# Kernel tuning notes

Hardware: AMD Instinct MI355X
Metric: run time of the kernel (lower is better)

The kernel has to match this reference:

```python
import jax, jax.numpy as jnp
import numpy as np
import math

BN_EPS = 1e-5
LOG20 = math.log(20.0)

def conv1x1(w, x):
    # w: [O, C], x: [B, C, N] -> [B, O, N]
    return jnp.einsum('oc,bcn->bon', w, x)

def bn_silu(x, g, b, m, v):
    # inference-mode BatchNorm1d over channel dim, then SiLU
    y = (x - m[None, :, None]) * (g / jnp.sqrt(v + BN_EPS))[None, :, None] + b[None, :, None]
    return y * jax.nn.sigmoid(y)

def setup_inputs() -> dict:
    key = jax.random.key(0)
    ks = jax.random.split(key, 16)
    B, N, M = 8, 4096, 4096
    f32 = jnp.float32
    d = {
        'pcd_f': jax.random.normal(ks[0], (B, 1152, N), f32),
        'img_f': jax.random.normal(ks[1], (B, 1024, M), f32),
        'q_w': jax.random.normal(ks[2], (1024, 1152), f32) * 0.02,
        'k_w': jax.random.normal(ks[3], (1024, 1024), f32) * 0.02,
        'v_w': jax.random.normal(ks[4], (1024, 1024), f32) * 0.02,
        'skip_w': jax.random.normal(ks[5], (1024, 1152), f32) * 0.02,
        'c1_w': jax.random.normal(ks[6], (256, 1024), f32) * 0.03,
        'bn1_g': jnp.ones((256,), f32),
        'bn1_b': jnp.zeros((256,), f32),
        'bn1_m': jax.random.normal(ks[7], (256,), f32) * 0.1,
        'bn1_v': jnp.ones((256,), f32) + 0.1 * jax.random.uniform(ks[8], (256,)),
        'c2_w': jax.random.normal(ks[9], (64, 256), f32) * 0.06,
        'bn2_g': jnp.ones((64,), f32),
        'bn2_b': jnp.zeros((64,), f32),
        'bn2_m': jax.random.normal(ks[10], (64,), f32) * 0.1,
        'bn2_v': jnp.ones((64,), f32) + 0.1 * jax.random.uniform(ks[11], (64,)),
        'c3_w': jax.random.normal(ks[12], (1, 64), f32) * 0.1,
        'c3_b': jnp.zeros((1,), f32),
    }
    return d

def reference(pcd_f, img_f, q_w, k_w, v_w, skip_w, c1_w, bn1_g, bn1_b, bn1_m, bn1_v,
              c2_w, bn2_g, bn2_b, bn2_m, bn2_v, c3_w, c3_b):
    q = conv1x1(q_w, pcd_f)                       # [B, 1024, N]
    k = conv1x1(k_w, img_f)                       # [B, 1024, M]
    v = conv1x1(v_w, img_f)                       # [B, 1024, M]
    scale = math.sqrt(q.shape[1])                 # sqrt(C) = 32
    energy = jnp.einsum('bcn,bcm->bnm', q, k) / scale
    attn = jax.nn.softmax(energy, axis=-1)        # [B, N, M]
    x = jnp.einsum('bnm,bcm->bcn', attn, v)       # [B, 1024, N]
    x = conv1x1(skip_w, pcd_f) + x
    x = bn_silu(conv1x1(c1_w, x), bn1_g, bn1_b, bn1_m, bn1_v)   # [B, 256, N]
    x = bn_silu(conv1x1(c2_w, x), bn2_g, bn2_b, bn2_m, bn2_v)   # [B, 64, N]
    x = conv1x1(c3_w, x) + c3_b[None, :, None]    # [B, 1, N]
    x = x[:, 0, :]                                # squeeze channel -> [B, N]
    return jax.nn.sigmoid(x * LOG20)              # 1/(1+20^-x)
```

## Files before the change

### kernel.cpp

```cpp
#include <hip/hip_runtime.h>

#define LOG20F 2.9957322735539909f
#define AS1 __attribute__((address_space(1)))
#define AS3 __attribute__((address_space(3)))

typedef __attribute__((ext_vector_type(4))) short short4v;
typedef __attribute__((ext_vector_type(8))) short short8;
typedef __attribute__((ext_vector_type(8))) __bf16 bf16x8;
typedef __attribute__((ext_vector_type(4))) float f32x4;

__device__ __forceinline__ short f2bf(float f) {
  unsigned u = __float_as_uint(f);
  u = u + 0x7fffu + ((u >> 16) & 1u);
  return (short)(u >> 16);
}
__device__ __forceinline__ float bf2f(short s) {
  return __uint_as_float(((unsigned)(unsigned short)s) << 16);
}

__device__ __forceinline__ void xcd_map(int& bx, int& by, int& bz) {
  int gx = gridDim.x, gy = gridDim.y;
  int nwg = gx * gy * (int)gridDim.z;
  int lin = bx + gx * (by + gy * bz);
  int q = nwg >> 3, r = nwg & 7;
  int xcd = lin & 7, idx = lin >> 3;
  int wg = (xcd < r ? xcd * (q + 1) : r * (q + 1) + (xcd - r) * q) + idx;
  int per_z = gx * gy;
  bz = wg / per_z;
  int rz = wg - bz * per_z;
  if ((gx & 3) == 0 && (gy & 3) == 0) {
    int nstx = gx >> 2;
    int st = rz >> 4, w = rz & 15;
    bx = ((st % nstx) << 2) + (w & 3);
    by = ((st / nstx) << 2) + (w >> 2);
  } else {
    bx = rz % gx;
    by = rz / gx;
  }
}

template <int EPI>
__global__ __launch_bounds__(512, 2) void gemm8(
    const short* __restrict__ A, const short* __restrict__ B,
    short* __restrict__ C, const short* __restrict__ addp,
    float* __restrict__ rs,
    int K, int lda, int ldb, int ldc, int ldadd,
    long abatch, long bbatch, long cbatch, long addbatch, float scale)
{
  __shared__ __align__(16) short lA[2][256 * 64];
  __shared__ __align__(16) short lB[2][256 * 64];
  __shared__ float rsum_l[256];

  int bx = blockIdx.x, by = blockIdx.y, bz = blockIdx.z;
  xcd_map(bx, by, bz);

  const int tid = threadIdx.x;
  const int lane = tid & 63, wid = tid >> 6;
  const int wr = wid >> 2, wc = wid & 3;

  const long bm = (long)bx * 256, bn = (long)by * 256;
  const short* Ab = A + (long)bz * abatch + bm * lda;
  const short* Bb = B + (long)bz * bbatch + bn * ldb;

  f32x4 acc[8][4] = {};

  const int NKT = K >> 6;

  auto stageA = [&](int buf, int kt) {
    int k0 = kt << 6;
#pragma unroll
    for (int i = 0; i < 4; ++i) {
      int idx = i * 512 + tid;
      int row = idx >> 3, ch = idx & 7;
      int chs = ch ^ (row & 7);
      __builtin_amdgcn_global_load_lds(
          (const AS1 void*)(Ab + (long)row * lda + k0 + chs * 8),
          (AS3 void*)(&lA[buf][row * 64 + ch * 8]), 16, 0, 0);
    }
  };
  auto stageB = [&](int buf, int kt) {
    int k0 = kt << 6;
#pragma unroll
    for (int i = 0; i < 4; ++i) {
      int idx = i * 512 + tid;
      int row = idx >> 3, ch = idx & 7;
      int chs = ch ^ (row & 7);
      __builtin_amdgcn_global_load_lds(
          (const AS1 void*)(Bb + (long)row * ldb + k0 + chs * 8),
          (AS3 void*)(&lB[buf][row * 64 + ch * 8]), 16, 0, 0);
    }
  };

  const int rr = lane & 15, cl = lane >> 4;
  bf16x8 bfr[4][2], af[4][2];

  auto loadA2 = [&](int buf, int h) {
#pragma unroll
    for (int f = 0; f < 4; ++f) {
      int row = wr * 128 + h * 64 + f * 16 + rr;
#pragma unroll
      for (int kk = 0; kk < 2; ++kk) {
        int pch = (kk * 4 + cl) ^ (row & 7);
        af[f][kk] = *(const bf16x8*)&lA[buf][row * 64 + pch * 8];
      }
    }
  };
  auto loadB2 = [&](int buf) {
#pragma unroll
    for (int ni = 0; ni < 4; ++ni) {
      int row = wc * 64 + ni * 16 + rr;
#pragma unroll
      for (int kk = 0; kk < 2; ++kk) {
        int pch = (kk * 4 + cl) ^ (row & 7);
        bfr[ni][kk] = *(const bf16x8*)&lB[buf][row * 64 + pch * 8];
      }
    }
  };

#define BAR() __builtin_amdgcn_s_barrier()
#define LGKM0() asm volatile("s_waitcnt lgkmcnt(0)" ::: "memory")
#define MFMA_H(h)                                                        \
  do {                                                                   \
    __builtin_amdgcn_s_setprio(1);                                       \
    _Pragma("unroll")                                                    \
    for (int f = 0; f < 4; ++f)                                          \
      _Pragma("unroll")                                                  \
      for (int ni = 0; ni < 4; ++ni)                                     \
        _Pragma("unroll")                                                \
        for (int kk = 0; kk < 2; ++kk)                                   \
          acc[(h) * 4 + f][ni] = __builtin_amdgcn_mfma_f32_16x16x32_bf16(\
              af[f][kk], bfr[ni][kk], acc[(h) * 4 + f][ni], 0, 0, 0);    \
    __builtin_amdgcn_s_setprio(0);                                       \
  } while (0)

  stageB(0, 0); stageA(0, 0); stageB(1, 1);
  asm volatile("s_waitcnt vmcnt(4)" ::: "memory");
  BAR();

  for (int t2 = 0; t2 < NKT; t2 += 2) {
    const bool more = (t2 + 2 < NKT);
    stageA(1, t2 + 1);
    loadB2(0); loadA2(0, 0);
    BAR(); LGKM0(); MFMA_H(0); BAR();
    if (more) stageB(0, t2 + 2);
    loadA2(0, 1);
    if (more) { asm volatile("s_waitcnt vmcnt(4)" ::: "memory"); }
    else      { asm volatile("s_waitcnt vmcnt(0)" ::: "memory"); }
    BAR(); LGKM0(); MFMA_H(1); BAR();
    if (more) stageA(0, t2 + 2);
    loadB2(1); loadA2(1, 0);
    BAR(); LGKM0(); MFMA_H(0); BAR();
    if (more) stageB(1, t2 + 3);
    loadA2(1, 1);
    if (more) { asm volatile("s_waitcnt vmcnt(4)" ::: "memory"); }
    else      { asm volatile("s_waitcnt vmcnt(0)" ::: "memory"); }
    BAR(); LGKM0(); MFMA_H(1); BAR();
  }
#undef BAR
#undef LGKM0
#undef MFMA_H

  if constexpr (EPI == 2) {
    if (tid < 256) rsum_l[tid] = 0.f;
    __syncthreads();
#pragma unroll
    for (int mi = 0; mi < 8; ++mi) {
      int lrow0 = wr * 128 + (mi >> 2) * 64 + (mi & 3) * 16 + (cl << 2);
#pragma unroll
      for (int r = 0; r < 4; ++r) {
        float part = 0.f;
#pragma unroll
        for (int ni = 0; ni < 4; ++ni) {
          long col = bn + wc * 64 + ni * 16 + rr;
          float e = __expf(acc[mi][ni][r] * scale);
          C[(long)bz * cbatch + (bm + lrow0 + r) * ldc + col] = f2bf(e);
          part += e;
        }
        part += __shfl_xor(part, 1);
        part += __shfl_xor(part, 2);
        part += __shfl_xor(part, 4);
        part += __shfl_xor(part, 8);
        if (rr == 0) atomicAdd(&rsum_l[lrow0 + r], part);
      }
    }
    __syncthreads();
    if (tid < 256) atomicAdd(&rs[(long)bz * 4096 + bm + tid], rsum_l[tid]);
  } else {
#pragma unroll
    for (int mi = 0; mi < 8; ++mi) {
      long row0 = bm + wr * 128 + (mi >> 2) * 64 + (mi & 3) * 16 + (cl << 2);
      float inv[4];
      if constexpr (EPI == 1) {
#pragma unroll
        for (int r = 0; r < 4; ++r)
          inv[r] = 1.f / rs[(long)bz * 4096 + row0 + r];
      }
#pragma unroll
      for (int ni = 0; ni < 4; ++ni) {
        long col = bn + wc * 64 + ni * 16 + rr;
#pragma unroll
        for (int r = 0; r < 4; ++r) {
          long off = (long)bz * cbatch + (row0 + r) * ldc + col;
          float v = acc[mi][ni][r] * scale;
          if constexpr (EPI == 1)
            v = v * inv[r] +
                bf2f(addp[(long)bz * addbatch + (row0 + r) * ldadd + col]);
          C[off] = f2bf(v);
        }
      }
    }
  }
}

__device__ __forceinline__ int swz32(int row, int ch) {
  return row * 32 + ((ch ^ ((row >> 1) & 3)) << 3);
}

template <int BM, int BN, int WR, int WC, int EPI>
__global__ __launch_bounds__(WR * WC * 64, 4) void gemm_bt(
    const short* __restrict__ A, const short* __restrict__ B,
    short* __restrict__ C, const short* __restrict__ addp,
    const float* __restrict__ sc, const float* __restrict__ sh,
    int K, int lda, int ldb, int ldc,
    long abatch, long bbatch, long cbatch, float scale)
{
  constexpr int NTH = WR * WC * 64;
  constexpr int WM = BM / WR, WN = BN / WC;
  constexpr int MR = WM / 16, NR = WN / 16;
  constexpr int CA = (BM * 4) / NTH, CB = (BN * 4) / NTH;

  __shared__ __align__(16) short lA[2][BM * 32];
  __shared__ __align__(16) short lB[2][BN * 32];

  int bx = blockIdx.x, by = blockIdx.y, bz = blockIdx.z;
  xcd_map(bx, by, bz);

  const int tid = threadIdx.x;
  const int lane = tid & 63, wid = tid >> 6;
  const int wr = wid / WC, wc = wid % WC;

  const long bm = (long)bx * BM, bn = (long)by * BN;
  const short* Ab = A + (long)bz * abatch + bm * lda;
  const short* Bb = B + (long)bz * bbatch + bn * ldb;

  f32x4 acc[MR][NR] = {};

  auto stage = [&](int buf, int k0) {
#pragma unroll
    for (int i = 0; i < CA; ++i) {
      int idx = i * NTH + tid, row = idx >> 2, ch = idx & 3;
      int chs = ch ^ ((row >> 1) & 3);
      __builtin_amdgcn_global_load_lds(
          (const AS1 void*)(Ab + (long)row * lda + k0 + chs * 8),
          (AS3 void*)(&lA[buf][idx * 8]), 16, 0, 0);
    }
#pragma unroll
    for (int i = 0; i < CB; ++i) {
      int idx = i * NTH + tid, row = idx >> 2, ch = idx & 3;
      int chs = ch ^ ((row >> 1) & 3);
      __builtin_amdgcn_global_load_lds(
          (const AS1 void*)(Bb + (long)row * ldb + k0 + chs * 8),
          (AS3 void*)(&lB[buf][idx * 8]), 16, 0, 0);
    }
  };

  const int NT = K >> 5;
  stage(0, 0);
  __syncthreads();
  int cur = 0;
  for (int t = 0; t < NT; ++t) {
    if (t + 1 < NT) stage(cur ^ 1, (t + 1) << 5);
    const int ch = lane >> 4, rrow = lane & 15;
    bf16x8 af[MR], bfr[NR];
#pragma unroll
    for (int mi = 0; mi < MR; ++mi) {
      int row = wr * WM + mi * 16 + rrow;
      af[mi] = *(const bf16x8*)&lA[cur][swz32(row, ch)];
    }
#pragma unroll
    for (int ni = 0; ni < NR; ++ni) {
      int row = wc * WN + ni * 16 + rrow;
      bfr[ni] = *(const bf16x8*)&lB[cur][swz32(row, ch)];
    }
    __builtin_amdgcn_s_setprio(1);
#pragma unroll
    for (int mi = 0; mi < MR; ++mi)
#pragma unroll
      for (int ni = 0; ni < NR; ++ni)
        acc[mi][ni] = __builtin_amdgcn_mfma_f32_16x16x32_bf16(
            af[mi], bfr[ni], acc[mi][ni], 0, 0, 0);
    __builtin_amdgcn_s_setprio(0);
    __syncthreads();
    cur ^= 1;
  }

#pragma unroll
  for (int mi = 0; mi < MR; ++mi) {
    long row0 = bm + wr * WM + mi * 16 + ((lane >> 4) << 2);
#pragma unroll
    for (int ni = 0; ni < NR; ++ni) {
      long col = bn + wc * WN + ni * 16 + (lane & 15);
#pragma unroll
      for (int r = 0; r < 4; ++r) {
        long off = (long)bz * cbatch + (row0 + r) * ldc + col;
        float v = acc[mi][ni][r] * scale;
        if constexpr (EPI == 1) v += bf2f(addp[off]);
        if constexpr (EPI == 2) {
          float y = v * sc[col] + sh[col];
          v = y / (1.f + __expf(-y));
        }
        C[off] = f2bf(v);
      }
    }
  }
}

__global__ __launch_bounds__(256) void transpose_cvt(
    const float* __restrict__ in, short* __restrict__ out, int C, int N)
{
  __shared__ float tile[32][33];
  int n0 = blockIdx.x * 32, c0 = blockIdx.y * 32;
  long z = (long)blockIdx.z * C * N;
  int tx = threadIdx.x & 31, ty = threadIdx.x >> 5;
#pragma unroll
  for (int r = 0; r < 4; ++r) {
    int cc = ty + r * 8;
    tile[cc][tx] = in[z + (long)(c0 + cc) * N + n0 + tx];
  }
  __syncthreads();
#pragma unroll
  for (int r = 0; r < 4; ++r) {
    int nn = ty + r * 8;
    out[z + (long)(n0 + nn) * C + c0 + tx] = f2bf(tile[tx][nn]);
  }
}

__global__ __launch_bounds__(256) void cvt_bf16(
    const float* __restrict__ in, short* __restrict__ out, long n)
{
  long i = ((long)blockIdx.x * 256 + threadIdx.x) * 4;
  if (i >= n) return;
  const float* p = in + i;
  short4v s;
  s[0] = f2bf(p[0]); s[1] = f2bf(p[1]); s[2] = f2bf(p[2]); s[3] = f2bf(p[3]);
  *(short4v*)(out + i) = s;
}

__global__ void bn_prep(const float* g1, const float* b1, const float* m1, const float* v1,
                        const float* g2, const float* b2, const float* m2, const float* v2,
                        float* s1, float* t1, float* s2, float* t2)
{
  int i = threadIdx.x;
  if (i < 256) { float s = g1[i] * rsqrtf(v1[i] + 1e-5f); s1[i] = s; t1[i] = b1[i] - m1[i] * s; }
  if (i < 64)  { float s = g2[i] * rsqrtf(v2[i] + 1e-5f); s2[i] = s; t2[i] = b2[i] - m2[i] * s; }
}

__global__ __launch_bounds__(256) void zerof(float* __restrict__ p, int n)
{
  int i = blockIdx.x * 256 + threadIdx.x;
  if (i < n) p[i] = 0.f;
}

__global__ __launch_bounds__(256) void c3_out(
    const short* __restrict__ y2, const float* __restrict__ w,
    const float* __restrict__ bias, float* __restrict__ o, int total)
{
  int i = blockIdx.x * 256 + threadIdx.x;
  if (i >= total) return;
  const short8* r = (const short8*)(y2 + (long)i * 64);
  float acc = 0.f;
#pragma unroll
  for (int j0 = 0; j0 < 8; ++j0) {
    short8 v = r[j0];
#pragma unroll
    for (int j = 0; j < 8; ++j) acc += bf2f(v[j]) * w[j0 * 8 + j];
  }
  acc += bias[0];
  float x = acc * LOG20F;
  o[i] = 1.f / (1.f + __expf(-x));
}

extern "C" void kernel_launch(void* const* d_in, const int* in_sizes, int n_in,
                              void* d_out, int out_size, void* d_ws, size_t ws_size,
                              hipStream_t stream) {
  const float* pcd  = (const float*)d_in[0];
  const float* img  = (const float*)d_in[1];
  const float* qw   = (const float*)d_in[2];
  const float* kw   = (const float*)d_in[3];
  const float* vw   = (const float*)d_in[4];
  const float* skw  = (const float*)d_in[5];
  const float* c1w  = (const float*)d_in[6];
  const float* bn1g = (const float*)d_in[7];
  const float* bn1b = (const float*)d_in[8];
  const float* bn1m = (const float*)d_in[9];
  const float* bn1v = (const float*)d_in[10];
  const float* c2w  = (const float*)d_in[11];
  const float* bn2g = (const float*)d_in[12];
  const float* bn2b = (const float*)d_in[13];
  const float* bn2m = (const float*)d_in[14];
  const float* bn2v = (const float*)d_in[15];
  const float* c3w  = (const float*)d_in[16];
  const float* c3b  = (const float*)d_in[17];
  float* out = (float*)d_out;

  char* ws = (char*)d_ws;
  const long QS  = 4096L * 1024;
  const long QS2 = 4096L * 2048;
  const long ES  = 4096L * 4096;
  const size_t ALGN = 256;
  auto align_up = [&](size_t x) { return (x + ALGN - 1) & ~(ALGN - 1); };

  size_t oPcd  = 0;
  size_t oImg  = align_up(oPcd + 8L * 4096 * 1152 * 2);
  size_t oQsk  = align_up(oImg + 8L * 4096 * 1024 * 2);
  size_t oKt   = align_up(oQsk + 8L * QS2 * 2);
  size_t oV    = align_up(oKt  + 8L * QS * 2);
  size_t oWqs  = align_up(oV   + 8L * QS * 2);
  size_t oWk   = align_up(oWqs + 2048L * 1152 * 2);
  size_t oWv   = align_up(oWk + 1024L * 1024 * 2);
  size_t oC1   = align_up(oWv + 1024L * 1024 * 2);
  size_t oC2   = align_up(oC1 + 256L * 1024 * 2);
  size_t oS1   = align_up(oC2 + 64L * 256 * 2);
  size_t oT1   = align_up(oS1 + 256 * 4);
  size_t oS2   = align_up(oT1 + 256 * 4);
  size_t oT2   = align_up(oS2 + 64 * 4);
  size_t oRs   = align_up(oT2 + 64 * 4);
  size_t oEnd  = align_up(oRs + 8L * 4096 * 4);

  short* pcdT  = (short*)(ws + oPcd);
  short* imgT  = (short*)(ws + oImg);
  short* qsk   = (short*)(ws + oQsk);
  short* kt    = (short*)(ws + oKt);
  short* vbuf  = (short*)(ws + oV);
  short* wqsk  = (short*)(ws + oWqs);
  short* wkb   = (short*)(ws + oWk);
  short* wvb   = (short*)(ws + oWv);
  short* c1b   = (short*)(ws + oC1);
  short* c2b   = (short*)(ws + oC2);
  float* s1 = (float*)(ws + oS1); float* t1 = (float*)(ws + oT1);
  float* s2 = (float*)(ws + oS2); float* t2 = (float*)(ws + oT2);
  float* rsum = (float*)(ws + oRs);

  int NB; short *attn, *xt;
  if (ws_size >= oEnd + (size_t)(8L * QS * 2)) {
    NB = 4; attn = (short*)(ws + 0); xt = (short*)(ws + oEnd);
  } else {
    NB = 2; attn = (short*)(ws + 0);
    xt = (short*)(ws + align_up((size_t)(2L * ES * 2)));
  }
  short* y1t = qsk;
  short* y2t = kt;

  cvt_bf16<<<dim3(1152), 256, 0, stream>>>(qw,  wqsk,                1024L * 1152);
  cvt_bf16<<<dim3(1152), 256, 0, stream>>>(skw, wqsk + 1024L * 1152, 1024L * 1152);
  cvt_bf16<<<dim3(1024), 256, 0, stream>>>(kw,  wkb,  1024L * 1024);
  cvt_bf16<<<dim3(1024), 256, 0, stream>>>(vw,  wvb,  1024L * 1024);
  cvt_bf16<<<dim3(256),  256, 0, stream>>>(c1w, c1b,  256L * 1024);
  cvt_bf16<<<dim3(16),   256, 0, stream>>>(c2w, c2b,  64L * 256);
  bn_prep<<<1, 256, 0, stream>>>(bn1g, bn1b, bn1m, bn1v, bn2g, bn2b, bn2m, bn2v,
                                 s1, t1, s2, t2);
  zerof<<<dim3(128), 256, 0, stream>>>(rsum, 8 * 4096);
  transpose_cvt<<<dim3(128, 36, 8), 256, 0, stream>>>(pcd, pcdT, 1152, 4096);
  transpose_cvt<<<dim3(128, 32, 8), 256, 0, stream>>>(img, imgT, 1024, 4096);

  gemm8<0><<<dim3(16, 8, 8), 512, 0, stream>>>(
      pcdT, wqsk, qsk, nullptr, nullptr,
      1152, 1152, 1152, 2048, 0, 4096L * 1152, 0, QS2, 0, 1.f);
  gemm8<0><<<dim3(16, 4, 8), 512, 0, stream>>>(
      imgT, wkb, kt, nullptr, nullptr,
      1024, 1024, 1024, 1024, 0, QS, 0, QS, 0, 1.f);
  gemm8<0><<<dim3(4, 16, 8), 512, 0, stream>>>(
      wvb, imgT, vbuf, nullptr, nullptr,
      1024, 1024, 1024, 4096, 0, 0, QS, QS, 0, 1.f);

  for (int b0 = 0; b0 < 8; b0 += NB) {
    gemm8<2><<<dim3(16, 16, NB), 512, 0, stream>>>(
        qsk + (long)b0 * QS2, kt + (long)b0 * QS, attn, nullptr,
        rsum + (long)b0 * 4096,
        1024, 2048, 1024, 4096, 0, QS2, QS, ES, 0, 0.03125f);
    gemm8<1><<<dim3(16, 4, NB), 512, 0, stream>>>(
        attn, vbuf + (long)b0 * QS, xt + (long)b0 * QS,
        qsk + (long)b0 * QS2 + 1024, rsum + (long)b0 * 4096,
        4096, 4096, 4096, 1024, 2048, ES, QS, QS, QS2, 1.f);
  }

  gemm_bt<128, 128, 2, 2, 2><<<dim3(32, 2, 8), 256, 0, stream>>>(
      xt, c1b, y1t, nullptr, s1, t1,
      1024, 1024, 1024, 256, QS, 0, 4096L * 256, 1.f);
  gemm_bt<128, 64, 4, 1, 2><<<dim3(32, 1, 8), 256, 0, stream>>>(
      y1t, c2b, y2t, nullptr, s2, t2,
      256, 256, 256, 64, 4096L * 256, 0, 4096L * 64, 1.f);
  c3_out<<<dim3(128), 256, 0, stream>>>(y2t, c3w, c3b, out, 32768);

  (void)in_sizes; (void)n_in; (void)out_size; (void)ws_size;
}
```

Baseline: 1.047 ms.

## Split GEMM main loop into quarter phases and allow eight-batch attention chunks

Result: no change. 1.056 ms (+0.8%).

```diff
diff --git a/kernel.cpp b/kernel.cpp
--- a/kernel.cpp
+++ b/kernel.cpp
@@ -66,24 +66,26 @@
 
   const int NKT = K >> 6;
 
-  auto stageA = [&](int buf, int kt) {
+  auto stageA = [&](int buf, int kt, int half) {
     int k0 = kt << 6;
 #pragma unroll
-    for (int i = 0; i < 4; ++i) {
+    for (int i = 0; i < 2; ++i) {
       int idx = i * 512 + tid;
-      int row = idx >> 3, ch = idx & 7;
+      int rl = idx >> 3, ch = idx & 7;
+      int row = half * 128 + rl;
       int chs = ch ^ (row & 7);
       __builtin_amdgcn_global_load_lds(
           (const AS1 void*)(Ab + (long)row * lda + k0 + chs * 8),
           (AS3 void*)(&lA[buf][row * 64 + ch * 8]), 16, 0, 0);
     }
   };
-  auto stageB = [&](int buf, int kt) {
+  auto stageB = [&](int buf, int kt, int half) {
     int k0 = kt << 6;
 #pragma unroll
-    for (int i = 0; i < 4; ++i) {
+    for (int i = 0; i < 2; ++i) {
       int idx = i * 512 + tid;
-      int row = idx >> 3, ch = idx & 7;
+      int rl = idx >> 3, ch = idx & 7;
+      int row = half * 128 + rl;
       int chs = ch ^ (row & 7);
       __builtin_amdgcn_global_load_lds(
           (const AS1 void*)(Bb + (long)row * ldb + k0 + chs * 8),
@@ -92,12 +94,12 @@
   };
 
   const int rr = lane & 15, cl = lane >> 4;
-  bf16x8 bfr[4][2], af[4][2];
-
-  auto loadA2 = [&](int buf, int h) {
-#pragma unroll
-    for (int f = 0; f < 4; ++f) {
-      int row = wr * 128 + h * 64 + f * 16 + rr;
+  bf16x8 bfr[4][2], af[2][2];
+
+  auto loadA = [&](int buf, int q) {
+#pragma unroll
+    for (int f = 0; f < 2; ++f) {
+      int row = wr * 128 + q * 32 + f * 16 + rr;
 #pragma unroll
       for (int kk = 0; kk < 2; ++kk) {
         int pch = (kk * 4 + cl) ^ (row & 7);
@@ -105,7 +107,7 @@
       }
     }
   };
-  auto loadB2 = [&](int buf) {
+  auto loadB = [&](int buf) {
 #pragma unroll
     for (int ni = 0; ni < 4; ++ni) {
       int row = wc * 64 + ni * 16 + rr;
@@ -119,53 +121,66 @@
 
 #define BAR() __builtin_amdgcn_s_barrier()
 #define LGKM0() asm volatile("s_waitcnt lgkmcnt(0)" ::: "memory")
-#define MFMA_H(h)                                                        \
+#define MFMA_Q(q)                                                        \
   do {                                                                   \
     __builtin_amdgcn_s_setprio(1);                                       \
     _Pragma("unroll")                                                    \
-    for (int f = 0; f < 4; ++f)                                          \
+    for (int f = 0; f < 2; ++f)                                          \
       _Pragma("unroll")                                                  \
       for (int ni = 0; ni < 4; ++ni)                                     \
         _Pragma("unroll")                                                \
         for (int kk = 0; kk < 2; ++kk)                                   \
-          acc[(h) * 4 + f][ni] = __builtin_amdgcn_mfma_f32_16x16x32_bf16(\
-              af[f][kk], bfr[ni][kk], acc[(h) * 4 + f][ni], 0, 0, 0);    \
+          acc[(q) * 2 + f][ni] = __builtin_amdgcn_mfma_f32_16x16x32_bf16(\
+              af[f][kk], bfr[ni][kk], acc[(q) * 2 + f][ni], 0, 0, 0);    \
     __builtin_amdgcn_s_setprio(0);                                       \
   } while (0)
 
-  stageB(0, 0); stageA(0, 0); stageB(1, 1);
+  stageB(0, 0, 0); stageB(0, 0, 1);
+  stageA(0, 0, 0); stageA(0, 0, 1);
+  stageB(1, 1, 0); stageB(1, 1, 1);
   asm volatile("s_waitcnt vmcnt(4)" ::: "memory");
   BAR();
 
   for (int t2 = 0; t2 < NKT; t2 += 2) {
-    const bool more = (t2 + 2 < NKT);
-    stageA(1, t2 + 1);
-    loadB2(0); loadA2(0, 0);
-    BAR(); LGKM0(); MFMA_H(0); BAR();
-    if (more) stageB(0, t2 + 2);
-    loadA2(0, 1);
+    const bool more = (t2 + 4 <= NKT);
+    loadB(0); loadA(0, 0);
+    stageA(1, t2 + 1, 0); stageA(1, t2 + 1, 1);
+    BAR(); LGKM0(); MFMA_Q(0); BAR();
+    loadA(0, 1);
+    if (more) stageB(0, t2 + 2, 0);
+    BAR(); LGKM0(); MFMA_Q(1); BAR();
+    loadA(0, 2);
+    if (more) stageB(0, t2 + 2, 1);
+    BAR(); LGKM0(); MFMA_Q(2); BAR();
+    loadA(0, 3);
     if (more) { asm volatile("s_waitcnt vmcnt(4)" ::: "memory"); }
     else      { asm volatile("s_waitcnt vmcnt(0)" ::: "memory"); }
-    BAR(); LGKM0(); MFMA_H(1); BAR();
-    if (more) stageA(0, t2 + 2);
-    loadB2(1); loadA2(1, 0);
-    BAR(); LGKM0(); MFMA_H(0); BAR();
-    if (more) stageB(1, t2 + 3);
-    loadA2(1, 1);
+    BAR(); LGKM0(); MFMA_Q(3); BAR();
+    loadB(1); loadA(1, 0);
+    if (more) stageA(0, t2 + 2, 0);
+    BAR(); LGKM0(); MFMA_Q(0); BAR();
+    loadA(1, 1);
+    if (more) stageA(0, t2 + 2, 1);
+    BAR(); LGKM0(); MFMA_Q(1); BAR();
+    loadA(1, 2);
+    if (more) stageB(1, t2 + 3, 0);
+    BAR(); LGKM0(); MFMA_Q(2); BAR();
+    loadA(1, 3);
+    if (more) stageB(1, t2 + 3, 1);
     if (more) { asm volatile("s_waitcnt vmcnt(4)" ::: "memory"); }
     else      { asm volatile("s_waitcnt vmcnt(0)" ::: "memory"); }
-    BAR(); LGKM0(); MFMA_H(1); BAR();
+    BAR(); LGKM0(); MFMA_Q(3); BAR();
   }
 #undef BAR
 #undef LGKM0
-#undef MFMA_H
+#undef MFMA_Q
 
   if constexpr (EPI == 2) {
     if (tid < 256) rsum_l[tid] = 0.f;
     __syncthreads();
 #pragma unroll
     for (int mi = 0; mi < 8; ++mi) {
-      int lrow0 = wr * 128 + (mi >> 2) * 64 + (mi & 3) * 16 + (cl << 2);
+      int lrow0 = wr * 128 + (mi >> 1) * 32 + (mi & 1) * 16 + (cl << 2);
 #pragma unroll
       for (int r = 0; r < 4; ++r) {
         float part = 0.f;
@@ -188,7 +203,7 @@
   } else {
 #pragma unroll
     for (int mi = 0; mi < 8; ++mi) {
-      long row0 = bm + wr * 128 + (mi >> 2) * 64 + (mi & 3) * 16 + (cl << 2);
+      long row0 = bm + wr * 128 + (mi >> 1) * 32 + (mi & 1) * 16 + (cl << 2);
       float inv[4];
       if constexpr (EPI == 1) {
 #pragma unroll
@@ -442,7 +457,10 @@
   float* rsum = (float*)(ws + oRs);
 
   int NB; short *attn, *xt;
-  if (ws_size >= oEnd + (size_t)(8L * QS * 2)) {
+  if (ws_size >= oEnd + (size_t)(8L * ES * 2) + (size_t)(8L * QS * 2)) {
+    NB = 8; attn = (short*)(ws + oEnd);
+    xt = (short*)(ws + align_up(oEnd + (size_t)(8L * ES * 2)));
+  } else if (ws_size >= oEnd + (size_t)(8L * QS * 2)) {
     NB = 4; attn = (short*)(ws + 0); xt = (short*)(ws + oEnd);
   } else {
     NB = 2; attn = (short*)(ws + 0);
```
